# Kernel optimization log

Hardware: AMD Instinct MI355X
Metric: run time of the kernel (lower is better)

## Reference

```python
import jax, jax.numpy as jnp
import numpy as np

# Model dims (match init_kwargs / input_specs)
B, CIN, COUT = 32, 32, 64
H, W = 128, 128
KH, KW = 3, 3
MAXCN = 64                    # max entries in connect_nums_list
HO, WO = H - KH + 1, W - KW + 1   # padding=0, stride=1


def setup_inputs() -> dict:
    key = jax.random.key(0)
    k1, k2, k3, k4 = jax.random.split(key, 4)
    x = jax.random.normal(k1, (B, CIN, H, W), dtype=jnp.float32)
    # padded kernel bank: [out_channel, connection_slot, kh, kw]
    weights = jax.random.normal(k2, (COUT, MAXCN, KH, KW), dtype=jnp.float32)
    # per-pixel bias map per output channel (original inits zeros; random exercises it)
    bias = jax.random.normal(k3, (COUT, HO, WO), dtype=jnp.float32) * 0.1
    connect_nums = jax.random.randint(k4, (COUT,), 1, MAXCN + 1, dtype=jnp.int32)
    return {"x": x, "weights": weights, "bias": bias, "connect_nums": connect_nums}


def reference(x, weights, bias, connect_nums):
    O, J = weights.shape[0], weights.shape[1]
    # mask out kernel slots beyond each channel's connection count
    mask = (jnp.arange(J)[None, :] < connect_nums[:, None]).astype(weights.dtype)  # [O,J]
    # slot j reads input channel j % CIN; conv is linear, so fold duplicate-channel
    # kernels into one effective dense kernel [O, CIN, KH, KW]
    onehot = jax.nn.one_hot(jnp.arange(J) % CIN, CIN, dtype=weights.dtype)  # [J,C]
    kdense = jnp.einsum('ojhw,oj,jc->ochw', weights, mask, onehot)
    out = jax.lax.conv_general_dilated(
        x, kdense, window_strides=(1, 1), padding='VALID',
        dimension_numbers=('NCHW', 'OIHW', 'NCHW'))  # [B,O,HO,WO]
    return out + bias[None]
```

## Files before the change

kernel.cpp:

```cpp
#include <hip/hip_runtime.h>

#define B_    32
#define CIN   32
#define COUT  64
#define H_    128
#define W_    128
#define HO_   126
#define WO_   126
#define MAXCN 64

typedef __attribute__((ext_vector_type(8))) short short8;
typedef __attribute__((ext_vector_type(4))) float floatx4;

static __device__ __forceinline__ unsigned short f2bf(float f) {
    union { float f; unsigned u; } v; v.f = f;
    unsigned r = v.u + 0x7fff + ((v.u >> 16) & 1);
    return (unsigned short)(r >> 16);
}

__global__ void fold_bf16(const float* __restrict__ w,
                          const int* __restrict__ cn,
                          unsigned short* __restrict__ wk) {
    int idx = blockIdx.x * 256 + threadIdx.x;
    if (idx >= 9 * COUT * CIN) return;
    int c   = idx & 31;
    int oc  = (idx >> 5) & 63;
    int tap = idx >> 11;
    int n = cn[oc];
    float v = 0.0f;
    if (c < n)      v += w[(oc * MAXCN + c) * 9 + tap];
    if (c + 32 < n) v += w[(oc * MAXCN + c + 32) * 9 + tap];
    wk[idx] = f2bf(v);
}

__global__ __launch_bounds__(256)
void nchw_to_nhwc_bf16(const float* __restrict__ x,
                       unsigned short* __restrict__ xb) {
    __shared__ unsigned short tile[128 * 34];
    const int b = blockIdx.y, y = blockIdx.x;
    const int t = threadIdx.x;
    const int xi = t & 127, c0 = t >> 7;
    const float* xp = x + ((size_t)(b * CIN) * H_ + y) * W_;
    for (int c = c0; c < CIN; c += 2) {
        float v = xp[(size_t)c * (H_ * W_) + xi];
        tile[xi * 34 + c] = f2bf(v);
    }
    __syncthreads();
    unsigned short* op = xb + ((size_t)(b * H_ + y) * W_) * CIN;
    for (int k = t; k < W_ * CIN; k += 256) {
        int c = k & 31, x2 = k >> 5;
        op[k] = tile[x2 * 34 + c];
    }
}

__global__ __launch_bounds__(256)
void conv_mfma(const unsigned short* __restrict__ xb,
               const unsigned short* __restrict__ wk,
               const float* __restrict__ bias,
               float* __restrict__ out) {
    __shared__ __align__(16) unsigned short xs[18 * 18 * 32];
    __shared__ __align__(16) unsigned short ws[9 * 64 * 32];

    const int tile = blockIdx.x;
    const int b    = blockIdx.y;
    const int tx = tile & 7, ty = tile >> 3;
    const int x0 = tx * 16, y0 = ty * 16;
    const int tid = threadIdx.x;

    uint4* xs4 = (uint4*)xs;
    for (int idx = tid; idx < 1296; idx += 256) {
        int yy = idx / 72;
        int r  = idx - yy * 72;
        int xc = r >> 2;
        int cp = r & 3;
        int iy = y0 + yy; if (iy > H_ - 1) iy = H_ - 1;
        int ix = x0 + xc; if (ix > W_ - 1) ix = W_ - 1;
        const uint4* s = (const uint4*)(xb + (((size_t)b * H_ + iy) * W_ + ix) * CIN) + cp;
        xs4[idx] = *s;
    }
    uint4* ws4 = (uint4*)ws;
    const uint4* wk4 = (const uint4*)wk;
    for (int idx = tid; idx < 2304; idx += 256) ws4[idx] = wk4[idx];
    __syncthreads();

    const int w_id = tid >> 6;
    const int lane = tid & 63;
    const int quad = lane >> 4, l16 = lane & 15;

    floatx4 acc[4][4];
#pragma unroll
    for (int i = 0; i < 4; ++i)
#pragma unroll
        for (int t = 0; t < 4; ++t) acc[i][t] = (floatx4)0.0f;

#pragma unroll
    for (int kh = 0; kh < 3; ++kh) {
#pragma unroll
        for (int kw = 0; kw < 3; ++kw) {
            const int tap = kh * 3 + kw;
            short8 a[4], bf[4];
#pragma unroll
            for (int t = 0; t < 4; ++t)
                a[t] = *(const short8*)&ws[((tap * 64 + t * 16 + l16) * 32) + quad * 8];
#pragma unroll
            for (int i = 0; i < 4; ++i)
                bf[i] = *(const short8*)&xs[(((4 * w_id + i + kh) * 18 + l16 + kw) * 32) + quad * 8];
#pragma unroll
            for (int i = 0; i < 4; ++i)
#pragma unroll
                for (int t = 0; t < 4; ++t)
                    acc[i][t] = __builtin_amdgcn_mfma_f32_16x16x32_bf16(a[t], bf[i], acc[i][t], 0, 0, 0);
        }
    }

    const int col = x0 + l16;
#pragma unroll
    for (int i = 0; i < 4; ++i) {
        const int y = y0 + 4 * w_id + i;
        if (y >= HO_ || col >= WO_) continue;
#pragma unroll
        for (int t = 0; t < 4; ++t) {
#pragma unroll
            for (int r = 0; r < 4; ++r) {
                const int oc = t * 16 + quad * 4 + r;
                out[(((size_t)b * COUT + oc) * HO_ + y) * WO_ + col] =
                    acc[i][t][r] + bias[((size_t)oc * HO_ + y) * WO_ + col];
            }
        }
    }
}

__global__ void fold_kernel(const float* __restrict__ w,
                            const int* __restrict__ cn,
                            float* __restrict__ kd) {
    int idx = blockIdx.x * blockDim.x + threadIdx.x;
    if (idx >= COUT * CIN * 9) return;
    int t = idx % 9;
    int c = (idx / 9) % CIN;
    int o = idx / (9 * CIN);
    int n = cn[o];
    float v = 0.0f;
    if (c < n)      v += w[(o * MAXCN + c) * 9 + t];
    if (c + 32 < n) v += w[(o * MAXCN + c + 32) * 9 + t];
    kd[idx] = v;
}

__global__ __launch_bounds__(256)
void conv_kernel(const float* __restrict__ x,
                 const float* __restrict__ kd,
                 const float* __restrict__ bias,
                 float* __restrict__ out) {
    __shared__ __align__(16) float xsh[CIN * 18 * 20];
    __shared__ __align__(16) float wsh[16 * 289];
    const int b = blockIdx.z, ocg = blockIdx.y, tile = blockIdx.x;
    const int ty = tile >> 3, txx = tile & 7;
    const int y0 = ty * 16, x0 = txx * 16;
    const int tid = threadIdx.x;
    const float* xbp = x + (size_t)b * CIN * H_ * W_;
    for (int idx = tid; idx < CIN * 18 * 18; idx += 256) {
        int c = idx / 324, rem = idx - c * 324, r = rem / 18, col = rem - r * 18;
        int iy = y0 + r;   if (iy > H_ - 1) iy = H_ - 1;
        int ix = x0 + col; if (ix > W_ - 1) ix = W_ - 1;
        xsh[c * 360 + r * 20 + col] = xbp[(c * H_ + iy) * W_ + ix];
    }
    for (int idx = tid; idx < 16 * 288; idx += 256) {
        int oc = idx / 288, rr = idx - oc * 288;
        wsh[oc * 289 + rr] = kd[(ocg * 16 + oc) * 288 + rr];
    }
    __syncthreads();
    const int oc_l = tid & 15, pb = tid >> 4, pby = pb >> 2, pbx = pb & 3;
    float acc[4][4];
#pragma unroll
    for (int i = 0; i < 4; ++i)
#pragma unroll
        for (int j = 0; j < 4; ++j) acc[i][j] = 0.0f;
    const float* xp = &xsh[(pby * 4) * 20 + pbx * 4];
    const float* wp = &wsh[oc_l * 289];
    for (int c = 0; c < CIN; ++c) {
        float xr[6][6];
#pragma unroll
        for (int r = 0; r < 6; ++r) {
            const float* row = xp + c * 360 + r * 20;
            float4 v4 = *reinterpret_cast<const float4*>(row);
            float2 v2 = *reinterpret_cast<const float2*>(row + 4);
            xr[r][0] = v4.x; xr[r][1] = v4.y; xr[r][2] = v4.z;
            xr[r][3] = v4.w; xr[r][4] = v2.x; xr[r][5] = v2.y;
        }
        float wr[9];
#pragma unroll
        for (int t = 0; t < 9; ++t) wr[t] = wp[c * 9 + t];
#pragma unroll
        for (int kh = 0; kh < 3; ++kh)
#pragma unroll
            for (int kw = 0; kw < 3; ++kw) {
                const float wv = wr[kh * 3 + kw];
#pragma unroll
                for (int i = 0; i < 4; ++i)
#pragma unroll
                    for (int j = 0; j < 4; ++j)
                        acc[i][j] = fmaf(xr[i + kh][j + kw], wv, acc[i][j]);
            }
    }
    const int o = ocg * 16 + oc_l;
    const int yb = y0 + pby * 4, xq0 = x0 + pbx * 4;
    float* ob = out + ((size_t)(b * COUT + o)) * HO_ * WO_;
    const float* bb = bias + (size_t)o * HO_ * WO_;
#pragma unroll
    for (int i = 0; i < 4; ++i) {
        int y = yb + i;
        if (y >= HO_) continue;
#pragma unroll
        for (int j = 0; j < 4; ++j) {
            int xq = xq0 + j;
            if (xq >= WO_) continue;
            ob[y * WO_ + xq] = acc[i][j] + bb[y * WO_ + xq];
        }
    }
}

extern "C" void kernel_launch(void* const* d_in, const int* in_sizes, int n_in,
                              void* d_out, int out_size, void* d_ws, size_t ws_size,
                              hipStream_t stream) {
    const float* x    = (const float*)d_in[0];
    const float* w    = (const float*)d_in[1];
    const float* bias = (const float*)d_in[2];
    const int*   cn   = (const int*)d_in[3];
    float* out = (float*)d_out;

    const size_t XB_BYTES = (size_t)B_ * H_ * W_ * CIN * 2;
    const size_t WK_BYTES = (size_t)9 * COUT * CIN * 2;

    if (ws_size >= XB_BYTES + WK_BYTES) {
        unsigned short* xbuf = (unsigned short*)d_ws;
        unsigned short* wkb  = (unsigned short*)((char*)d_ws + XB_BYTES);
        fold_bf16<<<(9 * COUT * CIN + 255) / 256, 256, 0, stream>>>(w, cn, wkb);
        nchw_to_nhwc_bf16<<<dim3(H_, B_), 256, 0, stream>>>(x, xbuf);
        conv_mfma<<<dim3(64, B_), 256, 0, stream>>>(xbuf, wkb, bias, out);
    } else {
        float* kd = (float*)d_ws;
        fold_kernel<<<(COUT * CIN * 9 + 255) / 256, 256, 0, stream>>>(w, cn, kd);
        dim3 grid(64, 4, B_);
        conv_kernel<<<grid, 256, 0, stream>>>(x, kd, bias, out);
    }
}
```

Baseline: 278.3 us.

## Split conv output channels across blocks and vectorize NHWC transpose stores

```diff
diff --git a/kernel.cpp b/kernel.cpp
--- a/kernel.cpp
+++ b/kernel.cpp
@@ -36,20 +36,22 @@
 __global__ __launch_bounds__(256)
 void nchw_to_nhwc_bf16(const float* __restrict__ x,
                        unsigned short* __restrict__ xb) {
-    __shared__ unsigned short tile[128 * 34];
     const int b = blockIdx.y, y = blockIdx.x;
     const int t = threadIdx.x;
-    const int xi = t & 127, c0 = t >> 7;
-    const float* xp = x + ((size_t)(b * CIN) * H_ + y) * W_;
-    for (int c = c0; c < CIN; c += 2) {
-        float v = xp[(size_t)c * (H_ * W_) + xi];
-        tile[xi * 34 + c] = f2bf(v);
-    }
-    __syncthreads();
-    unsigned short* op = xb + ((size_t)(b * H_ + y) * W_) * CIN;
-    for (int k = t; k < W_ * CIN; k += 256) {
-        int c = k & 31, x2 = k >> 5;
-        op[k] = tile[x2 * 34 + c];
+    const int c8  = t & 3;
+    const int xi0 = t >> 2;
+    const float* xp = x + (size_t)b * CIN * H_ * W_ + (size_t)y * W_;
+#pragma unroll
+    for (int it = 0; it < 2; ++it) {
+        const int xi = xi0 + it * 64;
+        __align__(16) unsigned short v[8];
+#pragma unroll
+        for (int j = 0; j < 8; ++j) {
+            const int c = c8 * 8 + j;
+            v[j] = f2bf(xp[(size_t)c * (H_ * W_) + xi]);
+        }
+        *(uint4*)(xb + (((size_t)b * H_ + y) * W_ + xi) * CIN + c8 * 8) =
+            *(const uint4*)v;
     }
 }
 
@@ -59,10 +61,11 @@
                const float* __restrict__ bias,
                float* __restrict__ out) {
     __shared__ __align__(16) unsigned short xs[18 * 18 * 32];
-    __shared__ __align__(16) unsigned short ws[9 * 64 * 32];
+    __shared__ __align__(16) unsigned short ws[9 * 32 * 32];
 
     const int tile = blockIdx.x;
-    const int b    = blockIdx.y;
+    const int ocg  = blockIdx.y;
+    const int b    = blockIdx.z;
     const int tx = tile & 7, ty = tile >> 3;
     const int x0 = tx * 16, y0 = ty * 16;
     const int tid = threadIdx.x;
@@ -80,35 +83,41 @@
     }
     uint4* ws4 = (uint4*)ws;
     const uint4* wk4 = (const uint4*)wk;
-    for (int idx = tid; idx < 2304; idx += 256) ws4[idx] = wk4[idx];
+    for (int idx = tid; idx < 1152; idx += 256) {
+        int tap  = idx >> 7;
+        int rem  = idx & 127;
+        int oc_l = rem >> 2;
+        int cp   = rem & 3;
+        ws4[idx] = wk4[tap * 256 + (ocg * 32 + oc_l) * 4 + cp];
+    }
     __syncthreads();
 
     const int w_id = tid >> 6;
     const int lane = tid & 63;
     const int quad = lane >> 4, l16 = lane & 15;
 
-    floatx4 acc[4][4];
+    floatx4 acc[4][2];
 #pragma unroll
     for (int i = 0; i < 4; ++i)
 #pragma unroll
-        for (int t = 0; t < 4; ++t) acc[i][t] = (floatx4)0.0f;
+        for (int t = 0; t < 2; ++t) acc[i][t] = (floatx4)0.0f;
 
 #pragma unroll
     for (int kh = 0; kh < 3; ++kh) {
 #pragma unroll
         for (int kw = 0; kw < 3; ++kw) {
             const int tap = kh * 3 + kw;
-            short8 a[4], bf[4];
-#pragma unroll
-            for (int t = 0; t < 4; ++t)
-                a[t] = *(const short8*)&ws[((tap * 64 + t * 16 + l16) * 32) + quad * 8];
+            short8 a[2], bf[4];
+#pragma unroll
+            for (int t = 0; t < 2; ++t)
+                a[t] = *(const short8*)&ws[((tap * 32 + t * 16 + l16) * 32) + quad * 8];
 #pragma unroll
             for (int i = 0; i < 4; ++i)
                 bf[i] = *(const short8*)&xs[(((4 * w_id + i + kh) * 18 + l16 + kw) * 32) + quad * 8];
 #pragma unroll
             for (int i = 0; i < 4; ++i)
 #pragma unroll
-                for (int t = 0; t < 4; ++t)
+                for (int t = 0; t < 2; ++t)
                     acc[i][t] = __builtin_amdgcn_mfma_f32_16x16x32_bf16(a[t], bf[i], acc[i][t], 0, 0, 0);
         }
     }
@@ -119,10 +128,10 @@
         const int y = y0 + 4 * w_id + i;
         if (y >= HO_ || col >= WO_) continue;
 #pragma unroll
-        for (int t = 0; t < 4; ++t) {
+        for (int t = 0; t < 2; ++t) {
 #pragma unroll
             for (int r = 0; r < 4; ++r) {
-                const int oc = t * 16 + quad * 4 + r;
+                const int oc = ocg * 32 + t * 16 + quad * 4 + r;
                 out[(((size_t)b * COUT + oc) * HO_ + y) * WO_ + col] =
                     acc[i][t][r] + bias[((size_t)oc * HO_ + y) * WO_ + col];
             }
@@ -235,7 +244,7 @@
         unsigned short* wkb  = (unsigned short*)((char*)d_ws + XB_BYTES);
         fold_bf16<<<(9 * COUT * CIN + 255) / 256, 256, 0, stream>>>(w, cn, wkb);
         nchw_to_nhwc_bf16<<<dim3(H_, B_), 256, 0, stream>>>(x, xbuf);
-        conv_mfma<<<dim3(64, B_), 256, 0, stream>>>(xbuf, wkb, bias, out);
+        conv_mfma<<<dim3(64, 2, B_), 256, 0, stream>>>(xbuf, wkb, bias, out);
     } else {
         float* kd = (float*)d_ws;
         fold_kernel<<<(COUT * CIN * 9 + 255) / 256, 256, 0, stream>>>(w, cn, kd);
```

Result: faster. 268.1 us (-3.7%).
